# Kernel optimization log

Measured on AMD Instinct MI355X. Metric: run time of the kernel, lower is better.

## Reference

```python
import jax, jax.numpy as jnp
import numpy as np

B, N, E, H, D = 8, 1024, 512, 8, 64  # batch, tokens, embed, heads, dim_head


def setup_inputs() -> dict:
    key = jax.random.key(0)
    ks = jax.random.split(key, 12)
    f = lambda k, s: jax.random.normal(k, s, dtype=jnp.float32)
    return {
        "x": f(ks[0], (B, N, E)),
        "r_t": f(ks[1], (B, N, E)),
        "r_c": f(ks[2], (B, N, E)),
        "bias_time_e": f(ks[3], (H, D)) * 0.02,
        "bias_time_r": f(ks[4], (H, D)) * 0.02,
        "bias_channel_r": f(ks[5], (H, D)) * 0.02,
        "bias_channel_e": f(ks[6], (H, D)) * 0.02,
        "w_qkv": f(ks[7], (E, 3 * H * D)) * 0.02,   # to_qkv (no bias)
        "w_kr_t": f(ks[8], (E, H * D)) * 0.02,      # k_r_time_net (no bias)
        "w_kr_c": f(ks[9], (E, H * D)) * 0.02,      # k_r_channel_net (no bias)
        "w_out": f(ks[10], (H * D, E)) * 0.02,      # to_out Linear
        "b_out": f(ks[11], (E,)) * 0.02,
    }


def _rel_shift(x):
    # x: [i, j, b, h] -- TransformerXL relative shift along j
    i, j, b, h = x.shape
    zp = jnp.zeros((i, 1, b, h), x.dtype)
    xp = jnp.concatenate([zp, x], axis=1).reshape(j + 1, i, b, h)
    return xp[1:].reshape(i, j, b, h)


def reference(x, r_t, r_c, bias_time_e, bias_time_r, bias_channel_r, bias_channel_e,
              w_qkv, w_kr_t, w_kr_c, w_out, b_out):
    b, n, _ = x.shape
    to_nbhd = lambda t: t.reshape(b, n, H, D).transpose(1, 0, 2, 3)  # [n,b,h,d]
    q, k, v = jnp.split(x @ w_qkv, 3, axis=-1)
    q, k, v = to_nbhd(q), to_nbhd(k), to_nbhd(v)
    qb = q + bias_time_e  # broadcast [h,d] over [n,b,h,d]
    wr_t = to_nbhd(r_t @ w_kr_t)
    wr_c = to_nbhd(r_c @ w_kr_c)
    AC = jnp.einsum('ibhd,jbhd->ijbh', qb, k)
    BD_t = _rel_shift(jnp.einsum('ibhd,jbhd->ijbh', qb, wr_t))
    BD_c = _rel_shift(jnp.einsum('ibhd,jbhd->ijbh', qb, wr_c))
    dots = AC + (BD_t + BD_c) * 0.5
    # Faithful to torch: nn.Softmax(dim=-1) on [i,j,b,h] normalizes over HEADS.
    attn = jax.nn.softmax(dots, axis=-1)
    out = jnp.einsum('ijbh,jbhd->ibhd', attn, v)
    out = out.transpose(1, 0, 2, 3).reshape(b, n, H * D) @ w_out + b_out
    return out, attn.transpose(2, 3, 0, 1)  # ([b,n,E], [b,h,q,k])
```

## Files before the change

### kernel.cpp

```cpp
#include <hip/hip_runtime.h>
#include <hip/hip_fp16.h>


typedef _Float16 f16;
typedef f16 f16x4 __attribute__((ext_vector_type(4)));
typedef f16 f16x8 __attribute__((ext_vector_type(8)));
typedef float f32x4 __attribute__((ext_vector_type(4)));

#define MFMA16(a,b,c) __builtin_amdgcn_mfma_f32_16x16x32_f16((a),(b),(c),0,0,0)

static __device__ __forceinline__ size_t qpidx(int bh, int q, int d) {
  return ((((size_t)bh * 64 + (q >> 4)) * 2 + (d >> 5)) * 64 +
          ((q & 15) + (((d >> 3) & 3) << 4))) * 8 + (d & 7);
}
static __device__ __forceinline__ size_t vpidx(int bh, int d, int j) {
  return ((((size_t)bh * 4 + (d >> 4)) * 32 + (j >> 5)) * 64 +
          ((d & 15) + (((j >> 3) & 3) << 4))) * 8 + (j & 7);
}

__global__ __launch_bounds__(256) void kprep(
    const float* __restrict__ x, const float* __restrict__ rt, const float* __restrict__ rc,
    const float* __restrict__ wqkv, const float* __restrict__ wkrt, const float* __restrict__ wkrc,
    f16* __restrict__ X16, f16* __restrict__ A2, f16* __restrict__ WQ, f16* __restrict__ W2)
{
  const int t = threadIdx.x, gx = blockIdx.x, mode = blockIdx.y;
  if (mode <= 2) {
    const size_t id = (size_t)gx * 256 + t;
    const float* src = (mode == 0) ? x : (mode == 1) ? rt : rc;
    float4 v0 = *(const float4*)&src[id * 8];
    float4 v1 = *(const float4*)&src[id * 8 + 4];
    f16x8 o = {(f16)v0.x, (f16)v0.y, (f16)v0.z, (f16)v0.w,
               (f16)v1.x, (f16)v1.y, (f16)v1.z, (f16)v1.w};
    if (mode == 0) *(f16x8*)&X16[id * 8] = o;
    else {
      const int mrow = (int)(id >> 6), cc = (int)(id & 63);
      *(f16x8*)&A2[(size_t)mrow * 1024 + (mode == 2 ? 512 : 0) + cc * 8] = o;
    }
  } else if (mode == 3) {
    if (gx >= 384) return;
    const int c = gx & 63, n = (gx >> 6) * 256 + t;
    f16x8 o;
    #pragma unroll
    for (int e = 0; e < 8; ++e) o[e] = (f16)wqkv[(size_t)(c * 8 + e) * 1536 + n];
    *(f16x8*)&WQ[(size_t)n * 512 + c * 8] = o;
  } else {
    if (gx >= 128) return;
    const int c = gx & 63, n = (gx >> 6) * 256 + t;
    const float* src = (mode == 4) ? wkrt : wkrc;
    f16x8 o;
    #pragma unroll
    for (int e = 0; e < 8; ++e) o[e] = (f16)src[(size_t)(c * 8 + e) * 512 + n];
    *(f16x8*)&W2[(size_t)n * 1024 + (mode == 5 ? 512 : 0) + c * 8] = o;
  }
}

__global__ __launch_bounds__(256) void kproj(
    const f16* __restrict__ X16, const f16* __restrict__ A2,
    const f16* __restrict__ WQ, const f16* __restrict__ W2,
    const float* __restrict__ bias_te,
    f16* __restrict__ QP, f16* __restrict__ KP, f16* __restrict__ VP, f16* __restrict__ WP)
{
  __shared__ f16 As[128 * 64];
  __shared__ f16 Bs[128 * 64];
  const int t = threadIdx.x, l = t & 63, w = t >> 6;
  const int wr = w >> 1, wc = w & 1;
  const int m0 = blockIdx.x * 128;
  const int y = blockIdx.y;
  const int mode = y >> 2;
  const bool wrs = (mode == 3);
  const f16* Asrc = wrs ? A2 : X16;
  const int lda = wrs ? 1024 : 512;
  const int K = wrs ? 1024 : 512;
  const f16* Bsrc = wrs ? (W2 + (size_t)((y - 12) * 128) * 1024)
                        : (WQ + (size_t)(y * 128) * 512);
  const int ldb = wrs ? 1024 : 512;

  f32x4 acc[4][4] = {};
  for (int k0 = 0; k0 < K; k0 += 64) {
    __syncthreads();
    #pragma unroll
    for (int rep = 0; rep < 4; ++rep) {
      const int idx = rep * 256 + t;
      const int row = idx >> 3, kb = idx & 7;
      const int slot = (kb ^ (row & 7)) << 3;
      f16x8 va = *(const f16x8*)&Asrc[(size_t)(m0 + row) * lda + k0 + kb * 8];
      *(f16x8*)&As[row * 64 + slot] = va;
      f16x8 vb = *(const f16x8*)&Bsrc[(size_t)row * ldb + k0 + kb * 8];
      *(f16x8*)&Bs[row * 64 + slot] = vb;
    }
    __syncthreads();
    #pragma unroll
    for (int kc = 0; kc < 2; ++kc) {
      f16x8 af[4], bf[4];
      const int kb = kc * 4 + (l >> 4);
      #pragma unroll
      for (int mb = 0; mb < 4; ++mb) {
        const int r = wr * 64 + mb * 16 + (l & 15);
        af[mb] = *(const f16x8*)&As[r * 64 + ((kb ^ (r & 7)) << 3)];
      }
      #pragma unroll
      for (int nb = 0; nb < 4; ++nb) {
        const int r = wc * 64 + nb * 16 + (l & 15);
        bf[nb] = *(const f16x8*)&Bs[r * 64 + ((kb ^ (r & 7)) << 3)];
      }
      #pragma unroll
      for (int mb = 0; mb < 4; ++mb)
      #pragma unroll
      for (int nb = 0; nb < 4; ++nb)
        acc[mb][nb] = MFMA16(af[mb], bf[nb], acc[mb][nb]);
    }
  }
  #pragma unroll
  for (int mb = 0; mb < 4; ++mb)
  #pragma unroll
  for (int nb = 0; nb < 4; ++nb) {
    const int loc = wc * 64 + nb * 16 + (l & 15);
    const int c = (y & 3) * 128 + loc;
    const int hh = c >> 6, d = c & 63;
    const float badd = (mode == 0) ? bias_te[c] : 0.f;
    f32x4 a = acc[mb][nb];
    #pragma unroll
    for (int r = 0; r < 4; ++r) {
      const int m = m0 + wr * 64 + mb * 16 + (l >> 4) * 4 + r;
      const int bb = m >> 10, tn = m & 1023;
      const int bh = bb * 8 + hh;
      const float v = a[r] + badd;
      if (mode == 0)      QP[qpidx(bh, tn, d)] = (f16)v;
      else if (mode == 1) KP[qpidx(bh, tn, d)] = (f16)v;
      else if (mode == 2) VP[vpidx(bh, d, tn)] = (f16)v;
      else                WP[qpidx(bh, tn, d)] = (f16)v;
    }
  }
}

__global__ __launch_bounds__(512, 4) void kdots(
    const f16* __restrict__ QP, const f16* __restrict__ KP,
    const f16* __restrict__ WP, const f16* __restrict__ VP,
    float* __restrict__ attn_out, float* __restrict__ OUTP)
{
  __shared__ f16 sd[8][32][72];
  const int t = threadIdx.x, l = t & 63, h = t >> 6;
  const int kg = blockIdx.x;
  const int q0 = blockIdx.y * 32;
  const int b = blockIdx.z;
  const int bh = b * 8 + h;
  const f16x8* QP8 = (const f16x8*)QP;
  const f16x8* KP8 = (const f16x8*)KP;
  const f16x8* WP8 = (const f16x8*)WP;
  const f16x8* VP8 = (const f16x8*)VP;
  const int qrow = (l >> 4) * 4;
  f16x8 aq[3][2];
  #pragma unroll
  for (int mb = 0; mb < 3; ++mb)
  #pragma unroll
  for (int kc = 0; kc < 2; ++kc)
    aq[mb][kc] = QP8[((size_t)(bh * 64 + (q0 >> 4) + mb) * 2 + kc) * 64 + l];

  f32x4 oacc[2][4] = {};

  for (int kti = 0; kti < 4; ++kti) {
    const int k0 = (kg * 4 + kti) * 64;
    {
      f32x4 acc[2][4] = {};
      #pragma unroll
      for (int kc = 0; kc < 2; ++kc) {
        #pragma unroll
        for (int nb = 0; nb < 4; ++nb) {
          f16x8 bf = KP8[((size_t)(bh * 64 + (k0 >> 4) + nb) * 2 + kc) * 64 + l];
          #pragma unroll
          for (int mb = 0; mb < 2; ++mb)
            acc[mb][nb] = MFMA16(aq[mb][kc], bf, acc[mb][nb]);
        }
      }
      #pragma unroll
      for (int mb = 0; mb < 2; ++mb)
      #pragma unroll
      for (int nb = 0; nb < 4; ++nb)
      #pragma unroll
      for (int r = 0; r < 4; ++r)
        sd[h][mb * 16 + qrow + r][nb * 16 + (l & 15)] = (f16)acc[mb][nb][r];
    }
    const int u0 = k0 - q0;
    auto rawblock = [&](int jb) {
      f32x4 racc[3] = {};
      #pragma unroll
      for (int kc = 0; kc < 2; ++kc) {
        f16x8 bf = WP8[((size_t)(bh * 64 + jb) * 2 + kc) * 64 + l];
        #pragma unroll
        for (int mb = 0; mb < 3; ++mb)
          racc[mb] = MFMA16(aq[mb][kc], bf, racc[mb]);
      }
      const int jglob = jb * 16 + (l & 15);
      #pragma unroll
      for (int mb = 0; mb < 3; ++mb)
      #pragma unroll
      for (int r = 0; r < 4; ++r) {
        const int qloc = mb * 16 + qrow + r;
        const int a = q0 + qloc;
        const float v = 0.5f * racc[mb][r];
        if (qloc < 32) {
          const int kA = a + jglob - 1023;
          if (kA >= k0 && kA < k0 + 64) {
            f16& s = sd[h][qloc][kA - k0];
            s = (f16)((float)s + v);
          }
        }
        if (qloc >= 1 && qloc <= 32) {
          const int kB = a + jglob + 1;
          if (kB >= k0 && kB < k0 + 64) {
            f16& s = sd[h][qloc - 1][kB - k0];
            s = (f16)((float)s + v);
          }
        }
      }
    };
    {
      const int blo_e = u0 - 33, bhi_e = (u0 + 61 > 1023) ? 1023 : u0 + 61;
      if (bhi_e >= 0) {
        const int blo = (blo_e < 0 ? 0 : blo_e) >> 4, bhi = bhi_e >> 4;
        for (int jb = blo; jb <= bhi; ++jb) rawblock(jb);
      }
      if (u0 <= 31) {
        const int alo_e = 992 + u0, ahi_e = (1086 + u0 > 1023) ? 1023 : 1086 + u0;
        const int alo = (alo_e < 0 ? 0 : alo_e) >> 4, ahi = ahi_e >> 4;
        for (int jb = alo; jb <= ahi; ++jb) rawblock(jb);
      }
    }
    __syncthreads();
    {
      const int o = t * 4, q = o >> 6, k = o & 63;
      float dv[8][4];
      #pragma unroll
      for (int hh = 0; hh < 8; ++hh) {
        f16x4 v = *(const f16x4*)&sd[hh][q][k];
        dv[hh][0] = (float)v[0]; dv[hh][1] = (float)v[1];
        dv[hh][2] = (float)v[2]; dv[hh][3] = (float)v[3];
      }
      #pragma unroll
      for (int e = 0; e < 4; ++e) {
        float m = dv[0][e];
        #pragma unroll
        for (int hh = 1; hh < 8; ++hh) m = fmaxf(m, dv[hh][e]);
        float ssum = 0.f;
        #pragma unroll
        for (int hh = 0; hh < 8; ++hh) { float a = __expf(dv[hh][e] - m); dv[hh][e] = a; ssum += a; }
        float rinv = 1.f / ssum;
        #pragma unroll
        for (int hh = 0; hh < 8; ++hh) dv[hh][e] *= rinv;
      }
      const size_t qg = q0 + q;
      #pragma unroll
      for (int hh = 0; hh < 8; ++hh) {
        f32x4* dst = (f32x4*)&attn_out[((size_t)(b * 8 + hh) * 1024 + qg) * 1024 + k0 + k];
        __builtin_nontemporal_store(f32x4{dv[hh][0], dv[hh][1], dv[hh][2], dv[hh][3]}, dst);
        *(f16x4*)&sd[hh][q][k] =
            f16x4{(f16)dv[hh][0], (f16)dv[hh][1], (f16)dv[hh][2], (f16)dv[hh][3]};
      }
    }
    __syncthreads();
    #pragma unroll
    for (int kc = 0; kc < 2; ++kc) {
      f16x8 pa[2];
      #pragma unroll
      for (int mb = 0; mb < 2; ++mb) {
        const int qq = mb * 16 + (l & 15);
        const int jj = kc * 32 + (l >> 4) * 8;
        pa[mb] = *(const f16x8*)&sd[h][qq][jj];
      }
      #pragma unroll
      for (int nb = 0; nb < 4; ++nb) {
        f16x8 vb = VP8[(((size_t)bh * 4 + nb) * 32 + (k0 >> 5) + kc) * 64 + l];
        #pragma unroll
        for (int mb = 0; mb < 2; ++mb)
          oacc[mb][nb] = MFMA16(pa[mb], vb, oacc[mb][nb]);
      }
    }
  }
  float* op = OUTP + ((size_t)kg * 8192 + (size_t)b * 1024) * 512;
  #pragma unroll
  for (int mb = 0; mb < 2; ++mb)
  #pragma unroll
  for (int nb = 0; nb < 4; ++nb)
  #pragma unroll
  for (int r = 0; r < 4; ++r) {
    const int qg = q0 + mb * 16 + qrow + r;
    const int dd = nb * 16 + (l & 15);
    op[(size_t)qg * 512 + h * 64 + dd] = oacc[mb][nb][r];
  }
}

__global__ __launch_bounds__(256) void kout(
    const float* __restrict__ OUTP, const float* __restrict__ w_out,
    const float* __restrict__ b_out, float* __restrict__ out)
{
  __shared__ f16 a_s[128][36];
  __shared__ f16 b_s[64][36];
  const int t = threadIdx.x, l = t & 63, w = t >> 6;
  const int m0 = blockIdx.x * 128;
  const int c0 = blockIdx.y * 64;
  f32x4 acc[2][4] = {};
  for (int k0 = 0; k0 < 512; k0 += 32) {
    __syncthreads();
    #pragma unroll
    for (int rep = 0; rep < 4; ++rep) {
      const int s = rep * 256 + t;
      const int r = s >> 3, c = (s & 7) * 4;
      const size_t off = (size_t)(m0 + r) * 512 + k0 + c;
      float4 v0 = *(const float4*)&OUTP[off];
      float4 v1 = *(const float4*)&OUTP[off + 4194304];
      float4 v2 = *(const float4*)&OUTP[off + 8388608];
      float4 v3 = *(const float4*)&OUTP[off + 12582912];
      *(f16x4*)&a_s[r][c] = f16x4{(f16)(v0.x + v1.x + v2.x + v3.x),
                                  (f16)(v0.y + v1.y + v2.y + v3.y),
                                  (f16)(v0.z + v1.z + v2.z + v3.z),
                                  (f16)(v0.w + v1.w + v2.w + v3.w)};
    }
    #pragma unroll
    for (int rep = 0; rep < 2; ++rep) {
      int idx = rep * 1024 + t * 4;
      int kr = idx >> 6, c = idx & 63;
      float4 v = *(const float4*)&w_out[(size_t)(k0 + kr) * 512 + c0 + c];
      b_s[c + 0][kr] = (f16)v.x; b_s[c + 1][kr] = (f16)v.y;
      b_s[c + 2][kr] = (f16)v.z; b_s[c + 3][kr] = (f16)v.w;
    }
    __syncthreads();
    const int kc = (l >> 4) * 8;
    f16x8 af[2];
    #pragma unroll
    for (int mb = 0; mb < 2; ++mb) {
      int r = w * 32 + mb * 16 + (l & 15);
      af[mb] = __builtin_shufflevector(*(const f16x4*)&a_s[r][kc], *(const f16x4*)&a_s[r][kc + 4],
                                       0, 1, 2, 3, 4, 5, 6, 7);
    }
    #pragma unroll
    for (int nb = 0; nb < 4; ++nb) {
      int cc = nb * 16 + (l & 15);
      f16x8 bf = __builtin_shufflevector(*(const f16x4*)&b_s[cc][kc], *(const f16x4*)&b_s[cc][kc + 4],
                                         0, 1, 2, 3, 4, 5, 6, 7);
      #pragma unroll
      for (int mb = 0; mb < 2; ++mb)
        acc[mb][nb] = MFMA16(af[mb], bf, acc[mb][nb]);
    }
  }
  #pragma unroll
  for (int mb = 0; mb < 2; ++mb)
  #pragma unroll
  for (int nb = 0; nb < 4; ++nb) {
    const int cg = c0 + nb * 16 + (l & 15);
    const float bb = b_out[cg];
    #pragma unroll
    for (int r = 0; r < 4; ++r) {
      const int m = m0 + w * 32 + mb * 16 + (l >> 4) * 4 + r;
      out[(size_t)m * 512 + cg] = acc[mb][nb][r] + bb;
    }
  }
}

extern "C" void kernel_launch(void* const* d_in, const int* in_sizes, int n_in,
                              void* d_out, int out_size, void* d_ws, size_t ws_size,
                              hipStream_t stream) {
  const float* x       = (const float*)d_in[0];
  const float* rt      = (const float*)d_in[1];
  const float* rc      = (const float*)d_in[2];
  const float* bias_te = (const float*)d_in[3];
  const float* w_qkv   = (const float*)d_in[7];
  const float* w_kr_t  = (const float*)d_in[8];
  const float* w_kr_c  = (const float*)d_in[9];
  const float* w_out   = (const float*)d_in[10];
  const float* b_out   = (const float*)d_in[11];
  float* out = (float*)d_out;
  float* attn_out = out + (size_t)8 * 1024 * 512;

  const size_t oX16 = 0;
  const size_t oA2  = oX16 + 4194304;
  const size_t oWQ  = oA2  + 8388608;
  const size_t oW2  = oWQ  + 786432;
  const size_t oQP  = oW2  + 524288;
  const size_t oKP  = oQP  + 4194304;
  const size_t oVP  = oKP  + 4194304;
  const size_t oWP  = oVP  + 4194304;
  const size_t oOP  = oWP  + 4194304;
  const size_t NEEDED = oOP * 2 + (size_t)4 * 8192 * 512 * 4;
  if (ws_size < NEEDED) return;
  f16* ws = (f16*)d_ws;
  f16 *X16 = ws + oX16, *A2 = ws + oA2, *WQ = ws + oWQ, *W2 = ws + oW2;
  f16 *QP = ws + oQP, *KP = ws + oKP, *VP = ws + oVP, *WP = ws + oWP;
  float* OUTP = (float*)(ws + oOP);

  kprep<<<dim3(2048, 6), 256, 0, stream>>>(x, rt, rc, w_qkv, w_kr_t, w_kr_c,
                                           X16, A2, WQ, W2);
  kproj<<<dim3(64, 16), 256, 0, stream>>>(X16, A2, WQ, W2, bias_te, QP, KP, VP, WP);
  kdots<<<dim3(4, 32, 8), 512, 0, stream>>>(QP, KP, WP, VP, attn_out, OUTP);
  kout<<<dim3(64, 8), 256, 0, stream>>>(OUTP, w_out, b_out, out);
}
```

Baseline: 229.6 us.

## Store partial attention outputs in fp16 and remap block indices for L2 locality

The partial per-key-group attention outputs written by kdots and summed in kout are stored as fp16 instead of fp32, halving that intermediate buffer's write and read traffic. kout loads them as 8-wide fp16 vectors and sums in fp32. Both kproj and kdots also remap their linear block index so consecutive blocks share weight tiles or batches, aiming at better cache reuse across the chiplets. The fp16 partials lose some precision before reduction.

```diff
diff --git a/kernel.cpp b/kernel.cpp
--- a/kernel.cpp
+++ b/kernel.cpp
@@ -64,8 +64,11 @@
   __shared__ f16 Bs[128 * 64];
   const int t = threadIdx.x, l = t & 63, w = t >> 6;
   const int wr = w >> 1, wc = w & 1;
-  const int m0 = blockIdx.x * 128;
-  const int y = blockIdx.y;
+  const int lin = blockIdx.x + 64 * blockIdx.y;
+  const int mchunk = lin & 7;
+  const int rem = lin >> 3;
+  const int m0 = (mchunk * 8 + (rem & 7)) * 128;
+  const int y = rem >> 3;
   const int mode = y >> 2;
   const bool wrs = (mode == 3);
   const f16* Asrc = wrs ? A2 : X16;
@@ -136,13 +139,15 @@
 __global__ __launch_bounds__(512, 4) void kdots(
     const f16* __restrict__ QP, const f16* __restrict__ KP,
     const f16* __restrict__ WP, const f16* __restrict__ VP,
-    float* __restrict__ attn_out, float* __restrict__ OUTP)
+    float* __restrict__ attn_out, f16* __restrict__ OUTP)
 {
   __shared__ f16 sd[8][32][72];
   const int t = threadIdx.x, l = t & 63, h = t >> 6;
-  const int kg = blockIdx.x;
-  const int q0 = blockIdx.y * 32;
-  const int b = blockIdx.z;
+  const int lin = blockIdx.x + 4 * blockIdx.y + 128 * blockIdx.z;
+  const int b = lin & 7;
+  const int rem = lin >> 3;
+  const int kg = rem & 3;
+  const int q0 = (rem >> 2) * 32;
   const int bh = b * 8 + h;
   const f16x8* QP8 = (const f16x8*)QP;
   const f16x8* KP8 = (const f16x8*)KP;
@@ -276,7 +281,7 @@
       }
     }
   }
-  float* op = OUTP + ((size_t)kg * 8192 + (size_t)b * 1024) * 512;
+  f16* op = OUTP + ((size_t)kg * 8192 + (size_t)b * 1024) * 512;
   #pragma unroll
   for (int mb = 0; mb < 2; ++mb)
   #pragma unroll
@@ -285,12 +290,12 @@
   for (int r = 0; r < 4; ++r) {
     const int qg = q0 + mb * 16 + qrow + r;
     const int dd = nb * 16 + (l & 15);
-    op[(size_t)qg * 512 + h * 64 + dd] = oacc[mb][nb][r];
+    op[(size_t)qg * 512 + h * 64 + dd] = (f16)oacc[mb][nb][r];
   }
 }
 
 __global__ __launch_bounds__(256) void kout(
-    const float* __restrict__ OUTP, const float* __restrict__ w_out,
+    const f16* __restrict__ OUTP, const float* __restrict__ w_out,
     const float* __restrict__ b_out, float* __restrict__ out)
 {
   __shared__ f16 a_s[128][36];
@@ -302,18 +307,22 @@
   for (int k0 = 0; k0 < 512; k0 += 32) {
     __syncthreads();
     #pragma unroll
-    for (int rep = 0; rep < 4; ++rep) {
+    for (int rep = 0; rep < 2; ++rep) {
       const int s = rep * 256 + t;
-      const int r = s >> 3, c = (s & 7) * 4;
+      const int r = s >> 2, c = (s & 3) * 8;
       const size_t off = (size_t)(m0 + r) * 512 + k0 + c;
-      float4 v0 = *(const float4*)&OUTP[off];
-      float4 v1 = *(const float4*)&OUTP[off + 4194304];
-      float4 v2 = *(const float4*)&OUTP[off + 8388608];
-      float4 v3 = *(const float4*)&OUTP[off + 12582912];
-      *(f16x4*)&a_s[r][c] = f16x4{(f16)(v0.x + v1.x + v2.x + v3.x),
-                                  (f16)(v0.y + v1.y + v2.y + v3.y),
-                                  (f16)(v0.z + v1.z + v2.z + v3.z),
-                                  (f16)(v0.w + v1.w + v2.w + v3.w)};
+      f16x8 p0 = *(const f16x8*)&OUTP[off];
+      f16x8 p1 = *(const f16x8*)&OUTP[off + 4194304];
+      f16x8 p2 = *(const f16x8*)&OUTP[off + 8388608];
+      f16x8 p3 = *(const f16x8*)&OUTP[off + 12582912];
+      f16x4 lo, hi;
+      #pragma unroll
+      for (int e = 0; e < 4; ++e) {
+        lo[e] = (f16)((float)p0[e] + (float)p1[e] + (float)p2[e] + (float)p3[e]);
+        hi[e] = (f16)((float)p0[e+4] + (float)p1[e+4] + (float)p2[e+4] + (float)p3[e+4]);
+      }
+      *(f16x4*)&a_s[r][c]     = lo;
+      *(f16x4*)&a_s[r][c + 4] = hi;
     }
     #pragma unroll
     for (int rep = 0; rep < 2; ++rep) {
@@ -380,12 +389,12 @@
   const size_t oVP  = oKP  + 4194304;
   const size_t oWP  = oVP  + 4194304;
   const size_t oOP  = oWP  + 4194304;
-  const size_t NEEDED = oOP * 2 + (size_t)4 * 8192 * 512 * 4;
+  const size_t NEEDED = (oOP + (size_t)4 * 8192 * 512) * 2;
   if (ws_size < NEEDED) return;
   f16* ws = (f16*)d_ws;
   f16 *X16 = ws + oX16, *A2 = ws + oA2, *WQ = ws + oWQ, *W2 = ws + oW2;
   f16 *QP = ws + oQP, *KP = ws + oKP, *VP = ws + oVP, *WP = ws + oWP;
-  float* OUTP = (float*)(ws + oOP);
+  f16* OUTP = ws + oOP;
 
   kprep<<<dim3(2048, 6), 256, 0, stream>>>(x, rt, rc, w_qkv, w_kr_t, w_kr_c,
                                            X16, A2, WQ, W2);
```

Result: no change. 233.2 us (+1.5%).
